# Kernel optimization log

Hardware: AMD Instinct MI355X
Metric: run time of the kernel (lower is better)

Reference implementation:

```python
import jax, jax.numpy as jnp
import numpy as np

L, KV, H, D, DM, F, V = 6, 1, 4, 256, 1152, 6912, 65536
HIST, T = 4095, 1
EPS = 1e-6


def setup_inputs():
    key = jax.random.key(0)
    ks = jax.random.split(key, 24)
    n = lambda k, s, sc=0.02: jax.random.normal(k, s, dtype=jnp.float32) * sc
    sf = D ** -0.25  # head_dim^-0.25 baked into q/k norm weights as in the source
    return {
        "input_ids": jax.random.randint(ks[0], (1, T), 0, V, dtype=jnp.int32),
        "attn_flag": 0,  # decode step: additive causal mask zeroed, as in the repo
        "key_cache": n(ks[1], (L, KV, D, HIST), 0.5),
        "value_cache": n(ks[2], (L, KV, HIST, D), 0.5),
        "embed_table": jax.random.randint(ks[3], (V, DM), 0, 256, dtype=jnp.int32),
        "embed_scale": jax.random.uniform(ks[4], (V, 1), minval=1e-4, maxval=1e-2, dtype=jnp.float32),
        "embed_zp": -jax.random.uniform(ks[5], (V, 1), minval=0.0, maxval=0.5, dtype=jnp.float32),
        "w_in_ln": 1.0 + n(ks[6], (L, DM)),
        "w_q_norm": (1.0 + n(ks[7], (L, D))) * sf,
        "w_k_norm": (1.0 + n(ks[8], (L, D))) * sf,
        "Wq": n(ks[9], (L, DM, H * D)),
        "Wk": n(ks[10], (L, DM, KV * D)),
        "Wv": n(ks[11], (L, DM, KV * D)),
        "Wo": n(ks[12], (L, H * D, DM)),
        "w_post_attn_ln": 1.0 + n(ks[13], (L, DM)),
        "w_pre_ffn_ln": 1.0 + n(ks[14], (L, DM)),
        "w_post_ffn_ln": 1.0 + n(ks[15], (L, DM)),
        "Wg": n(ks[16], (L, DM, F)),
        "Wu": n(ks[17], (L, DM, F)),
        "Wd": n(ks[18], (L, F, DM)),
        "w_final_norm": 1.0 + n(ks[19], (DM,)),
        "W_lm": n(ks[20], (DM, V)),
        "is_sliding": (jnp.arange(L) % 6) != 5,  # 5 local : 1 global pattern
    }


def _rms(x, w):
    return w * x / jnp.sqrt(jnp.mean(x * x, axis=-1, keepdims=True) + EPS)


def _rot_half(x, axis):
    x1, x2 = jnp.split(x, 2, axis=axis)
    return jnp.concatenate([-x2, x1], axis=axis)


def _rope(base, hist, S, d):
    pos = jnp.arange(hist, S, dtype=jnp.float32)[:, None]
    theta = base ** (-(jnp.arange(0, d, 2, dtype=jnp.float32) / d))
    ang = pos * theta
    c = jnp.concatenate([jnp.cos(ang)] * 2, axis=-1).astype(jnp.float16).astype(jnp.float32)
    s = jnp.concatenate([jnp.sin(ang)] * 2, axis=-1).astype(jnp.float16).astype(jnp.float32)
    return c, s  # (T, D), half-precision roundtrip mimics the .half() tables


def reference(input_ids, attn_flag, key_cache, value_cache, embed_table, embed_scale,
              embed_zp, w_in_ln, w_q_norm, w_k_norm, Wq, Wk, Wv, Wo, w_post_attn_ln,
              w_pre_ffn_ln, w_post_ffn_ln, Wg, Wu, Wd, w_final_norm, W_lm, is_sliding):
    Lc, KVc, Dd, hist = key_cache.shape
    Tq = input_ids.shape[1]
    S = hist + Tq
    Hh = Wq.shape[-1] // Dd
    G = Hh // KVc
    cos_g, sin_g = _rope(10000.0, hist, S, Dd)    # assigned to 'global' exactly as in source
    cos_l, sin_l = _rope(1000000.0, hist, S, Dd)  # assigned to 'local'
    mask = (jnp.arange(S)[None, :] > jnp.arange(Tq)[:, None]).astype(jnp.float32) * (-128.0 * float(attn_flag))  # (T,S)
    # int8-dequant embedding lookup: uint8 codes * per-row scale + per-row zero point
    h = embed_table[input_ids].astype(jnp.float32) * embed_scale[input_ids] + embed_zp[input_ids]  # (1,T,DM)

    def body(h, xs):
        ck, cv, slide, w_in, w_qn, w_kn, wq, wk, wv, wo, w_pa, w_pf, w_pof, wg, wu, wd = xs
        cq = jnp.where(slide, cos_l, cos_g)
        sq = jnp.where(slide, sin_l, sin_g)
        ckk, skk = cq.T, sq.T  # (D,T) for keys
        resid = h
        hn = _rms(h, w_in)                                                  # (1,T,DM)
        q = _rms((hn @ wq).reshape(Tq, Hh, Dd), w_qn).transpose(1, 0, 2)    # (H,T,D)
        k = _rms((hn @ wk).reshape(Tq, KVc, Dd), w_kn).transpose(1, 2, 0)   # (KV,D,T)
        v = (hn @ wv).reshape(Tq, KVc, Dd).transpose(1, 0, 2)               # (KV,T,D)
        q = q * cq + _rot_half(q, -1) * sq
        k = k * ckk[None] + _rot_half(k, 1) * skk[None]
        kf = jnp.concatenate([ck, k], axis=-1)   # (KV,D,S) new key cache
        vf = jnp.concatenate([cv, v], axis=1)    # (KV,S,D) new value cache
        kr = jnp.repeat(kf, G, axis=0)           # GQA repeat -> (H,D,S)
        vr = jnp.repeat(vf, G, axis=0)           # (H,S,D)
        attn = jax.nn.softmax(jnp.einsum('htd,hds->hts', q, kr) + mask[None], axis=-1)
        ao = jnp.einsum('hts,hsd->htd', attn, vr).transpose(1, 0, 2).reshape(1, Tq, Hh * Dd) @ wo
        h = resid + _rms(ao, w_pa)
        resid = h
        x = _rms(h, w_pf)
        m = (jax.nn.gelu(x @ wg, approximate=True) * (x @ wu)) @ wd
        h = resid + _rms(m, w_pof)
        return h, (kf, vf)

    h, (keys, values) = jax.lax.scan(
        body, h,
        (key_cache, value_cache, is_sliding, w_in_ln, w_q_norm, w_k_norm, Wq, Wk, Wv, Wo,
         w_post_attn_ln, w_pre_ffn_ln, w_post_ffn_ln, Wg, Wu, Wd))
    last = _rms(h[:, -1], w_final_norm)          # (1,DM)
    logits = last @ W_lm                          # (1,V)
    token = jnp.argmax(logits, axis=-1, keepdims=True).astype(jnp.int32)
    return keys, values, token
```

## Files before the change

kernel.cpp:

```cpp
#include <hip/hip_runtime.h>
#include <hip/hip_fp16.h>
#include <cmath>

#define LNUM 6
#define DM   1152
#define DHEAD 256
#define NH   4
#define FF   6912
#define VOC  65536
#define HIST 4095
#define SEQ  4096
#define EPSV 1e-6f

#define QKV_O 0
#define AP_O  9216
#define DP_O  16128
#define GU_O  23040
#define LG_O  105984
#define ZEND  171520
#define POP_O 171520
#define SPS_O 302592
#define HIN_O 303104
#define HM_O  310016
#define AMV_O 316928
#define AMI_O 317184

__device__ __forceinline__ float block_sum256(float v, float* red4) {
#pragma unroll
    for (int off = 32; off; off >>= 1) v += __shfl_xor(v, off);
    int t = threadIdx.x;
    if ((t & 63) == 0) red4[t >> 6] = v;
    __syncthreads();
    float r = red4[0] + red4[1] + red4[2] + red4[3];
    __syncthreads();
    return r;
}

__global__ __launch_bounds__(256) void gk_copy(const float* __restrict__ kc,
                                               const float* __restrict__ vc,
                                               float* __restrict__ keys,
                                               float* __restrict__ vals) {
    int b = blockIdx.x;
    if (b < 24576) {
        int row = b >> 4;
        int s = ((b & 15) << 8) + threadIdx.x;
        if (s < HIST) keys[(size_t)row * SEQ + s] = kc[(size_t)row * HIST + s];
    } else {
        int r = (b - 24576) * 4 + (threadIdx.x >> 6);
        int d4 = threadIdx.x & 63;
        if (r < LNUM * HIST) {
            int l = r / HIST, sI = r - l * HIST;
            ((float4*)(vals + ((size_t)l * SEQ + sI) * DHEAD))[d4] =
                ((const float4*)(vc + (size_t)r * DHEAD))[d4];
        }
    }
}

__global__ __launch_bounds__(256) void gk_qkv(
    const float* __restrict__ Wq, const float* __restrict__ Wk, const float* __restrict__ Wv,
    const float* __restrict__ w_in, const float* __restrict__ w_pof_prev,
    const float* __restrict__ hprev, const float* __restrict__ dprev,
    const int* __restrict__ ids, const int* __restrict__ tbl,
    const float* __restrict__ escale, const float* __restrict__ ezp,
    float* __restrict__ hin_out, float* __restrict__ qkv_out, int has_prev) {
    __shared__ float xv[DM];
    __shared__ float red4[4];
    __shared__ float4 qred[256];
    int t = threadIdx.x;
    if (has_prev) {
        float ss = 0.f;
        for (int i = t; i < DM; i += 256) { float d = dprev[i]; ss += d * d; }
        ss = block_sum256(ss, red4);
        float inv = 1.f / sqrtf(ss / DM + EPSV);
        for (int i = t; i < DM; i += 256)
            xv[i] = hprev[i] + w_pof_prev[i] * dprev[i] * inv;
    } else {
        int tok = ids[0];
        float sc = escale[tok], z = ezp[tok];
        const int* row = tbl + (size_t)tok * DM;
        for (int i = t; i < DM; i += 256) xv[i] = (float)row[i] * sc + z;
    }
    __syncthreads();
    if (blockIdx.x == 0 && blockIdx.y == 0)
        for (int i = t; i < DM; i += 256) hin_out[i] = xv[i];
    float ss = 0.f;
    for (int i = t; i < DM; i += 256) { float v = xv[i]; ss += v * v; }
    ss = block_sum256(ss, red4);
    float inv = 1.f / sqrtf(ss / DM + EPSV);
    for (int i = t; i < DM; i += 256) xv[i] = w_in[i] * xv[i] * inv;
    __syncthreads();

    int f4c = t & 63, ks = t >> 6;
    int jf = blockIdx.x * 64 + f4c;
    const float4* W4; int jj4, ncol4;
    if (jf < 256)      { W4 = (const float4*)Wq; jj4 = jf;       ncol4 = 256; }
    else if (jf < 320) { W4 = (const float4*)Wk; jj4 = jf - 256; ncol4 = 64; }
    else               { W4 = (const float4*)Wv; jj4 = jf - 320; ncol4 = 64; }
    int i0 = blockIdx.y * 64 + ks * 16;
    float4 w[16];
#pragma unroll
    for (int r = 0; r < 16; ++r) w[r] = W4[(size_t)(i0 + r) * ncol4 + jj4];
    float4 acc = {0, 0, 0, 0};
#pragma unroll
    for (int r = 0; r < 16; ++r) {
        float xs = xv[i0 + r];
        acc.x += xs * w[r].x; acc.y += xs * w[r].y;
        acc.z += xs * w[r].z; acc.w += xs * w[r].w;
    }
    qred[t] = acc;
    __syncthreads();
    if (ks == 0) {
        float4 a = qred[f4c], b = qred[64 + f4c], c = qred[128 + f4c], d = qred[192 + f4c];
        atomicAdd(&qkv_out[4 * jf + 0], a.x + b.x + c.x + d.x);
        atomicAdd(&qkv_out[4 * jf + 1], a.y + b.y + c.y + d.y);
        atomicAdd(&qkv_out[4 * jf + 2], a.z + b.z + c.z + d.z);
        atomicAdd(&qkv_out[4 * jf + 3], a.w + b.w + c.w + d.w);
    }
}

__global__ __launch_bounds__(256) void gk_attn(
    const float* __restrict__ qkv, const float* __restrict__ w_qn,
    const float* __restrict__ w_kn, const int* __restrict__ attn_flag,
    float* __restrict__ keys_l, float* __restrict__ vals_l,
    float* __restrict__ po_part, float* __restrict__ sum_part, float rope_base) {
    __shared__ float lq[NH * DHEAD];
    __shared__ float lqf[NH * DHEAD];
    __shared__ float lkn[DHEAD];
    __shared__ float lkf[DHEAD];
    __shared__ float lv[DHEAD];
    __shared__ float lp[NH * 32];
    __shared__ float red4[4];
    int t = threadIdx.x;
    int s0 = blockIdx.x * 32;
    bool last = (blockIdx.x == gridDim.x - 1);

    int jm = t & 127;
    float theta = powf(rope_base, -(float)(2 * jm) / 256.f);
    float ang = 4095.f * theta;
    float c = __half2float(__float2half(cosf(ang)));
    float s = __half2float(__float2half(sinf(ang)));

    for (int h = 0; h < NH; ++h) lq[h * 256 + t] = qkv[h * 256 + t];
    lkn[t] = qkv[1024 + t];
    lv[t]  = qkv[1280 + t];
    __syncthreads();
    for (int h = 0; h < NH; ++h) {
        float v = lq[h * 256 + t];
        float ss = block_sum256(v * v, red4);
        float inv = 1.f / sqrtf(ss / 256.f + EPSV);
        float qn = w_qn[t] * v * inv;
        lq[h * 256 + t] = qn;
        __syncthreads();
        float partner = (t < 128) ? -lq[h * 256 + t + 128] : lq[h * 256 + t - 128];
        lqf[h * 256 + t] = qn * c + partner * s;
    }
    {
        float v = lkn[t];
        float ss = block_sum256(v * v, red4);
        float inv = 1.f / sqrtf(ss / 256.f + EPSV);
        float kn = w_kn[t] * v * inv;
        lkn[t] = kn;
        __syncthreads();
        float partner = (t < 128) ? -lkn[t + 128] : lkn[t - 128];
        lkf[t] = kn * c + partner * s;
    }
    __syncthreads();
    if (last) {
        keys_l[(size_t)t * SEQ + (SEQ - 1)] = lkf[t];
        vals_l[(size_t)(SEQ - 1) * DHEAD + t] = lv[t];
    }
    int sl = t & 31, dc = t >> 5;
    int sg = s0 + sl;
    bool self = last && (sl == 31);
    float a0 = 0, a1 = 0, a2 = 0, a3 = 0;
#pragma unroll 4
    for (int dd = 0; dd < 32; ++dd) {
        int d = dc * 32 + dd;
        float kv = self ? lkf[d] : keys_l[(size_t)d * SEQ + sg];
        a0 += lqf[0 * 256 + d] * kv;
        a1 += lqf[1 * 256 + d] * kv;
        a2 += lqf[2 * 256 + d] * kv;
        a3 += lqf[3 * 256 + d] * kv;
    }
    __syncthreads();
    lq[0 * 256 + t] = a0; lq[1 * 256 + t] = a1; lq[2 * 256 + t] = a2; lq[3 * 256 + t] = a3;
    __syncthreads();
    if (t < 32) {
        int af = attn_flag[0];
        float mk = (s0 + t > 0) ? -128.f * (float)af : 0.f;
        for (int h = 0; h < NH; ++h) {
            float sc_ = 0.f;
#pragma unroll
            for (int d8 = 0; d8 < 8; ++d8) sc_ += lq[h * 256 + d8 * 32 + t];
            lp[h * 32 + t] = expf(sc_ + mk);
        }
    }
    __syncthreads();
    if (t < NH) {
        float su = 0.f;
        for (int i = 0; i < 32; ++i) su += lp[t * 32 + i];
        sum_part[blockIdx.x * NH + t] = su;
    }
    float p0 = 0, p1 = 0, p2 = 0, p3 = 0;
#pragma unroll 4
    for (int ss_ = 0; ss_ < 32; ++ss_) {
        float v = (last && ss_ == 31) ? lv[t] : vals_l[(size_t)(s0 + ss_) * DHEAD + t];
        p0 += lp[0 * 32 + ss_] * v;
        p1 += lp[1 * 32 + ss_] * v;
        p2 += lp[2 * 32 + ss_] * v;
        p3 += lp[3 * 32 + ss_] * v;
    }
    float* po = po_part + (size_t)blockIdx.x * NH * DHEAD;
    po[0 * 256 + t] = p0; po[1 * 256 + t] = p1; po[2 * 256 + t] = p2; po[3 * 256 + t] = p3;
}

__global__ __launch_bounds__(256) void gk_wo(
    const float* __restrict__ po_part, const float* __restrict__ sum_part,
    const float* __restrict__ Wo_l, float* __restrict__ aproj) {
    __shared__ float x[64];
    __shared__ float hinv[NH];
    __shared__ float red4[4];
    int t = threadIdx.x;
    for (int h = 0; h < NH; ++h) {
        float v = (t < 128) ? sum_part[t * NH + h] : 0.f;
        float tot = block_sum256(v, red4);
        if (t == 0) hinv[h] = 1.f / tot;
    }
    __syncthreads();
    int i0 = blockIdx.y * 64;
    if (t < 64) {
        float a = 0.f;
#pragma unroll 8
        for (int b = 0; b < 128; ++b) a += po_part[(size_t)b * 1024 + i0 + t];
        x[t] = a * hinv[(i0 + t) >> 8];
    }
    __syncthreads();
    int j = blockIdx.x * 256 + t;
    if (j < DM) {
        float acc = 0.f;
#pragma unroll 4
        for (int ii = 0; ii < 64; ++ii)
            acc += x[ii] * Wo_l[(size_t)(i0 + ii) * DM + j];
        atomicAdd(&aproj[j], acc);
    }
}

__global__ __launch_bounds__(256) void gk_gu(
    const float* __restrict__ Wg_l, const float* __restrict__ Wu_l,
    const float* __restrict__ w_pa, const float* __restrict__ w_pf,
    const float* __restrict__ hin, const float* __restrict__ aproj,
    float* __restrict__ hmid_out, float* __restrict__ gu_out) {
    __shared__ float xv[DM];
    __shared__ float red4[4];
    __shared__ float4 gred[256];
    int t = threadIdx.x;
    float ss = 0.f;
    for (int i = t; i < DM; i += 256) { float a = aproj[i]; ss += a * a; }
    ss = block_sum256(ss, red4);
    float inv = 1.f / sqrtf(ss / DM + EPSV);
    for (int i = t; i < DM; i += 256) xv[i] = hin[i] + w_pa[i] * aproj[i] * inv;
    __syncthreads();
    if (blockIdx.x == 0 && blockIdx.y == 0)
        for (int i = t; i < DM; i += 256) hmid_out[i] = xv[i];
    float s2 = 0.f;
    for (int i = t; i < DM; i += 256) { float v = xv[i]; s2 += v * v; }
    s2 = block_sum256(s2, red4);
    float inv2 = 1.f / sqrtf(s2 / DM + EPSV);
    for (int i = t; i < DM; i += 256) xv[i] = w_pf[i] * xv[i] * inv2;
    __syncthreads();

    int f4c = t & 63, ks = t >> 6;
    int cgi = blockIdx.x;
    bool isU = cgi >= 27;
    int cg = isU ? cgi - 27 : cgi;
    const float4* W4 = (const float4*)(isU ? Wu_l : Wg_l);
    int colf4 = cg * 64 + f4c;
    int i0 = blockIdx.y * 64 + ks * 16;
    float4 w[16];
#pragma unroll
    for (int r = 0; r < 16; ++r) w[r] = W4[(size_t)(i0 + r) * 1728 + colf4];
    float4 acc = {0, 0, 0, 0};
#pragma unroll
    for (int r = 0; r < 16; ++r) {
        float xs = xv[i0 + r];
        acc.x += xs * w[r].x; acc.y += xs * w[r].y;
        acc.z += xs * w[r].z; acc.w += xs * w[r].w;
    }
    gred[t] = acc;
    __syncthreads();
    if (ks == 0) {
        float4 a = gred[f4c], b = gred[64 + f4c], c = gred[128 + f4c], d = gred[192 + f4c];
        float* dst = gu_out + (isU ? FF : 0) + 4 * colf4;
        atomicAdd(dst + 0, a.x + b.x + c.x + d.x);
        atomicAdd(dst + 1, a.y + b.y + c.y + d.y);
        atomicAdd(dst + 2, a.z + b.z + c.z + d.z);
        atomicAdd(dst + 3, a.w + b.w + c.w + d.w);
    }
}

__global__ __launch_bounds__(256) void gk_wd(const float* __restrict__ gu,
                                             const float* __restrict__ Wd_l,
                                             float* __restrict__ dproj) {
    __shared__ float m[64];
    __shared__ float4 wred[256];
    int t = threadIdx.x;
    int i0 = blockIdx.y * 64;
    if (t < 64) {
        float g = gu[i0 + t], u = gu[FF + i0 + t];
        float gl = 0.5f * g * (1.f + tanhf(0.7978845608028654f * (g + 0.044715f * g * g * g)));
        m[t] = gl * u;
    }
    __syncthreads();
    int f4c = t & 63, ks = t >> 6;
    int col4 = blockIdx.x * 64 + f4c;
    float4 acc = {0, 0, 0, 0};
    if (col4 < 288) {
        const float4* W4 = (const float4*)Wd_l;
        float4 w[16];
#pragma unroll
        for (int r = 0; r < 16; ++r) w[r] = W4[(size_t)(i0 + ks * 16 + r) * 288 + col4];
#pragma unroll
        for (int r = 0; r < 16; ++r) {
            float xs = m[ks * 16 + r];
            acc.x += xs * w[r].x; acc.y += xs * w[r].y;
            acc.z += xs * w[r].z; acc.w += xs * w[r].w;
        }
    }
    wred[t] = acc;
    __syncthreads();
    if (ks == 0 && col4 < 288) {
        float4 a = wred[f4c], b = wred[64 + f4c], c = wred[128 + f4c], d = wred[192 + f4c];
        atomicAdd(&dproj[4 * col4 + 0], a.x + b.x + c.x + d.x);
        atomicAdd(&dproj[4 * col4 + 1], a.y + b.y + c.y + d.y);
        atomicAdd(&dproj[4 * col4 + 2], a.z + b.z + c.z + d.z);
        atomicAdd(&dproj[4 * col4 + 3], a.w + b.w + c.w + d.w);
    }
}

__global__ __launch_bounds__(256) void gk_logits(
    const float* __restrict__ W_lm, const float* __restrict__ w_pof5,
    const float* __restrict__ w_fin, const float* __restrict__ hmid5,
    const float* __restrict__ dproj5, float* __restrict__ lg) {
    __shared__ float xv[DM];
    __shared__ float red4[4];
    __shared__ float4 lred[256];
    int t = threadIdx.x;
    float ss = 0.f;
    for (int i = t; i < DM; i += 256) { float d = dproj5[i]; ss += d * d; }
    ss = block_sum256(ss, red4);
    float inv = 1.f / sqrtf(ss / DM + EPSV);
    for (int i = t; i < DM; i += 256) xv[i] = hmid5[i] + w_pof5[i] * dproj5[i] * inv;
    __syncthreads();
    float s2 = 0.f;
    for (int i = t; i < DM; i += 256) { float v = xv[i]; s2 += v * v; }
    s2 = block_sum256(s2, red4);
    float inv2 = 1.f / sqrtf(s2 / DM + EPSV);
    for (int i = t; i < DM; i += 256) xv[i] = w_fin[i] * xv[i] * inv2;
    __syncthreads();

    int f4c = t & 63, ks = t >> 6;
    int colf4 = blockIdx.x * 64 + f4c;
    int i0 = blockIdx.y * 64 + ks * 16;
    const float4* W4 = (const float4*)W_lm;
    float4 w[16];
#pragma unroll
    for (int r = 0; r < 16; ++r) w[r] = W4[(size_t)(i0 + r) * 16384 + colf4];
    float4 acc = {0, 0, 0, 0};
#pragma unroll
    for (int r = 0; r < 16; ++r) {
        float xs = xv[i0 + r];
        acc.x += xs * w[r].x; acc.y += xs * w[r].y;
        acc.z += xs * w[r].z; acc.w += xs * w[r].w;
    }
    lred[t] = acc;
    __syncthreads();
    if (ks == 0) {
        float4 a = lred[f4c], b = lred[64 + f4c], c = lred[128 + f4c], d = lred[192 + f4c];
        atomicAdd(&lg[4 * colf4 + 0], a.x + b.x + c.x + d.x);
        atomicAdd(&lg[4 * colf4 + 1], a.y + b.y + c.y + d.y);
        atomicAdd(&lg[4 * colf4 + 2], a.z + b.z + c.z + d.z);
        atomicAdd(&lg[4 * colf4 + 3], a.w + b.w + c.w + d.w);
    }
}

__global__ __launch_bounds__(256) void gk_amax1(const float* __restrict__ lg,
                                                float* __restrict__ pv, float* __restrict__ pi) {
    __shared__ float rv[256];
    __shared__ int ri[256];
    int t = threadIdx.x;
    int c = blockIdx.x * 256 + t;
    rv[t] = lg[c]; ri[t] = c;
    __syncthreads();
    for (int off = 128; off > 0; off >>= 1) {
        if (t < off) {
            float ov = rv[t + off]; int oi = ri[t + off];
            if (ov > rv[t] || (ov == rv[t] && oi < ri[t])) { rv[t] = ov; ri[t] = oi; }
        }
        __syncthreads();
    }
    if (t == 0) { pv[blockIdx.x] = rv[0]; pi[blockIdx.x] = (float)ri[0]; }
}

__global__ __launch_bounds__(256) void gk_amax2(const float* __restrict__ pv,
                                                const float* __restrict__ pi,
                                                float* __restrict__ tok_out) {
    __shared__ float rv[256];
    __shared__ int ri[256];
    int t = threadIdx.x;
    rv[t] = pv[t]; ri[t] = (int)pi[t];
    __syncthreads();
    for (int off = 128; off > 0; off >>= 1) {
        if (t < off) {
            float ov = rv[t + off]; int oi = ri[t + off];
            if (ov > rv[t] || (ov == rv[t] && oi < ri[t])) { rv[t] = ov; ri[t] = oi; }
        }
        __syncthreads();
    }
    if (t == 0) tok_out[0] = (float)ri[0];
}

extern "C" void kernel_launch(void* const* d_in, const int* in_sizes, int n_in,
                              void* d_out, int out_size, void* d_ws, size_t ws_size,
                              hipStream_t stream) {
    const int*   ids   = (const int*)d_in[0];
    const int*   aflag = (const int*)d_in[1];
    const float* kc    = (const float*)d_in[2];
    const float* vc    = (const float*)d_in[3];
    const int*   tbl   = (const int*)d_in[4];
    const float* esc   = (const float*)d_in[5];
    const float* ezp   = (const float*)d_in[6];
    const float* w_in  = (const float*)d_in[7];
    const float* w_qn  = (const float*)d_in[8];
    const float* w_kn  = (const float*)d_in[9];
    const float* Wq    = (const float*)d_in[10];
    const float* Wk    = (const float*)d_in[11];
    const float* Wv    = (const float*)d_in[12];
    const float* Wo    = (const float*)d_in[13];
    const float* w_pa  = (const float*)d_in[14];
    const float* w_pf  = (const float*)d_in[15];
    const float* w_pof = (const float*)d_in[16];
    const float* Wg    = (const float*)d_in[17];
    const float* Wu    = (const float*)d_in[18];
    const float* Wd    = (const float*)d_in[19];
    const float* w_fin = (const float*)d_in[20];
    const float* Wlm   = (const float*)d_in[21];

    float* keys = (float*)d_out;
    float* vals = keys + (size_t)LNUM * DHEAD * SEQ;
    float* tok  = vals + (size_t)LNUM * SEQ * DHEAD;
    float* ws = (float*)d_ws;

    hipMemsetAsync(ws, 0, ZEND * sizeof(float), stream);
    gk_copy<<<24576 + 6144, 256, 0, stream>>>(kc, vc, keys, vals);

    for (int l = 0; l < LNUM; ++l) {
        float* QKVl = ws + QKV_O + (size_t)l * 1536;
        float* APl  = ws + AP_O + (size_t)l * DM;
        float* DPl  = ws + DP_O + (size_t)l * DM;
        float* GUl  = ws + GU_O + (size_t)l * 2 * FF;
        float* HINl = ws + HIN_O + (size_t)l * DM;
        float* HMl  = ws + HM_O + (size_t)l * DM;
        float* keys_l = keys + (size_t)l * DHEAD * SEQ;
        float* vals_l = vals + (size_t)l * SEQ * DHEAD;

        gk_qkv<<<dim3(6, 18), 256, 0, stream>>>(
            Wq + (size_t)l * DM * 1024, Wk + (size_t)l * DM * 256,
            Wv + (size_t)l * DM * 256, w_in + (size_t)l * DM,
            w_pof + (size_t)(l ? l - 1 : 0) * DM,
            (l ? ws + HM_O + (size_t)(l - 1) * DM : nullptr),
            (l ? ws + DP_O + (size_t)(l - 1) * DM : nullptr),
            ids, tbl, esc, ezp, HINl, QKVl, (l > 0) ? 1 : 0);

        gk_attn<<<128, 256, 0, stream>>>(
            QKVl, w_qn + (size_t)l * DHEAD, w_kn + (size_t)l * DHEAD,
            aflag, keys_l, vals_l, ws + POP_O, ws + SPS_O,
            ((l % 6) != 5) ? 1000000.0f : 10000.0f);

        gk_wo<<<dim3(5, 16), 256, 0, stream>>>(
            ws + POP_O, ws + SPS_O, Wo + (size_t)l * 1024 * DM, APl);

        gk_gu<<<dim3(54, 18), 256, 0, stream>>>(
            Wg + (size_t)l * DM * FF, Wu + (size_t)l * DM * FF,
            w_pa + (size_t)l * DM, w_pf + (size_t)l * DM, HINl, APl, HMl, GUl);

        gk_wd<<<dim3(5, 108), 256, 0, stream>>>(GUl, Wd + (size_t)l * FF * DM, DPl);
    }

    gk_logits<<<dim3(256, 18), 256, 0, stream>>>(
        Wlm, w_pof + (size_t)5 * DM, w_fin,
        ws + HM_O + (size_t)5 * DM, ws + DP_O + (size_t)5 * DM, ws + LG_O);
    gk_amax1<<<256, 256, 0, stream>>>(ws + LG_O, ws + AMV_O, ws + AMI_O);
    gk_amax2<<<1, 256, 0, stream>>>(ws + AMV_O, ws + AMI_O, tok);
}
```

Measured before the change: 579.1 us.

## Fuse whole decode step into one cooperative persistent kernel with grid syncs

Replaces the sequence of about 33 kernel launches plus a memset with a single cooperative kernel of 256 blocks by 512 threads. Stages are separated by grid-wide barriers. The KV-cache copy for the next layer runs in idle blocks while attention executes, and the argmax is done with a packed 64-bit atomicMax. This removes launch gaps and lets the cache copy overlap compute. In exchange, every stage is limited to 256 blocks and pays grid-sync latency, and the old multi-kernel path is kept as a fallback if the cooperative launch fails.

```diff
diff --git a/kernel.cpp b/kernel.cpp
--- a/kernel.cpp
+++ b/kernel.cpp
@@ -1,6 +1,9 @@
 #include <hip/hip_runtime.h>
 #include <hip/hip_fp16.h>
+#include <hip/hip_cooperative_groups.h>
 #include <cmath>
+
+namespace cg = cooperative_groups;
 
 #define LNUM 6
 #define DM   1152
@@ -11,19 +14,477 @@
 #define HIST 4095
 #define SEQ  4096
 #define EPSV 1e-6f
+#define NB   256
+#define BS   512
 
 #define QKV_O 0
 #define AP_O  9216
 #define DP_O  16128
 #define GU_O  23040
 #define LG_O  105984
-#define ZEND  171520
-#define POP_O 171520
-#define SPS_O 302592
-#define HIN_O 303104
-#define HM_O  310016
-#define AMV_O 316928
-#define AMI_O 317184
+#define AMX_O 171520
+#define ZEND  171522
+#define POP_O 171528
+#define SPS_O 302600
+#define HIN_O 303112
+#define HM_O  310024
+#define AMV_O 316936
+#define AMI_O 317192
+
+struct P {
+    const int* ids; const int* aflag;
+    const float* kc; const float* vc;
+    const int* tbl; const float* esc; const float* ezp;
+    const float* w_in; const float* w_qn; const float* w_kn;
+    const float* Wq; const float* Wk; const float* Wv; const float* Wo;
+    const float* w_pa; const float* w_pf; const float* w_pof;
+    const float* Wg; const float* Wu; const float* Wd;
+    const float* w_fin; const float* Wlm;
+    float* keys; float* vals; float* tok; float* ws;
+};
+
+__device__ __forceinline__ float bsum512(float v, float* red8) {
+#pragma unroll
+    for (int off = 32; off; off >>= 1) v += __shfl_xor(v, off);
+    if ((threadIdx.x & 63) == 0) red8[threadIdx.x >> 6] = v;
+    __syncthreads();
+    float r = red8[0] + red8[1] + red8[2] + red8[3] +
+              red8[4] + red8[5] + red8[6] + red8[7];
+    __syncthreads();
+    return r;
+}
+
+__device__ __forceinline__ void copy_layer(const P& p, int l, int part) {
+    int t = threadIdx.x;
+#pragma unroll
+    for (int rr = 0; rr < 2; ++rr) {
+        int row = part * 2 + rr;
+        const float* src = p.kc + ((size_t)l * 256 + row) * HIST;
+        float* dst = p.keys + ((size_t)l * 256 + row) * SEQ;
+        for (int s = t; s < HIST; s += BS) dst[s] = src[s];
+    }
+    const float4* vc4 = (const float4*)p.vc;
+    float4* va4 = (float4*)p.vals;
+#pragma unroll
+    for (int rr = 0; rr < 4; ++rr) {
+        int s = part * 32 + rr * 8 + (t >> 6);
+        if (s < HIST)
+            va4[((size_t)l * SEQ + s) * 64 + (t & 63)] =
+                vc4[((size_t)l * HIST + s) * 64 + (t & 63)];
+    }
+}
+
+__global__ __launch_bounds__(BS) void mega(P p) {
+    cg::grid_group gg = cg::this_grid();
+    __shared__ float sm[5632];
+    const int t = threadIdx.x, bid = blockIdx.x;
+    float* ws = p.ws;
+
+    {
+        for (int g = bid * BS + t; g < ZEND; g += NB * BS) ws[g] = 0.f;
+        if (bid == 0) {
+            int tk = p.ids[0];
+            float sc = p.esc[tk], z = p.ezp[tk];
+            const int* row = p.tbl + (size_t)tk * DM;
+            for (int i = t; i < DM; i += BS) ws[HIN_O + i] = (float)row[i] * sc + z;
+        }
+        if (bid < 128) copy_layer(p, 0, bid);
+    }
+    gg.sync();
+
+    for (int l = 0; l < LNUM; ++l) {
+        float* QKV = ws + QKV_O + l * 1536;
+        float* AP  = ws + AP_O + l * DM;
+        float* DP  = ws + DP_O + l * DM;
+        float* GU  = ws + GU_O + l * 13824;
+        float* HIN = ws + HIN_O + l * DM;
+        float* HM  = ws + HM_O + l * DM;
+        float* POP = ws + POP_O;
+        float* SPS = ws + SPS_O;
+        float* keys_l = p.keys + (size_t)l * DHEAD * SEQ;
+        float* vals_l = p.vals + (size_t)l * SEQ * DHEAD;
+
+        {
+            float* xv = sm; float* red8 = sm + 1152;
+            float4* qred = (float4*)(sm + 1216);
+            if (l == 0) {
+                for (int i = t; i < DM; i += BS) xv[i] = ws[HIN_O + i];
+            } else {
+                const float* hprev = ws + HM_O + (l - 1) * DM;
+                const float* dprev = ws + DP_O + (l - 1) * DM;
+                const float* wpof = p.w_pof + (l - 1) * DM;
+                float ssd = 0.f;
+                for (int i = t; i < DM; i += BS) { float d = dprev[i]; ssd += d * d; }
+                ssd = bsum512(ssd, red8);
+                float inv = 1.f / sqrtf(ssd / DM + EPSV);
+                for (int i = t; i < DM; i += BS)
+                    xv[i] = hprev[i] + wpof[i] * dprev[i] * inv;
+            }
+            __syncthreads();
+            if (bid == 0) for (int i = t; i < DM; i += BS) HIN[i] = xv[i];
+            float ss2 = 0.f;
+            for (int i = t; i < DM; i += BS) { float v = xv[i]; ss2 += v * v; }
+            ss2 = bsum512(ss2, red8);
+            float inv2 = 1.f / sqrtf(ss2 / DM + EPSV);
+            const float* w_in = p.w_in + l * DM;
+            for (int i = t; i < DM; i += BS) xv[i] = w_in[i] * xv[i] * inv2;
+            __syncthreads();
+            if (bid < 96) {
+                int cg = bid % 6, kc = bid / 6;
+                int f4c = t & 63, ks = t >> 6;
+                int jf = cg * 64 + f4c;
+                const float4* W4; int jj4, nc4;
+                if (jf < 256)      { W4 = (const float4*)(p.Wq + (size_t)l * DM * 1024); jj4 = jf;       nc4 = 256; }
+                else if (jf < 320) { W4 = (const float4*)(p.Wk + (size_t)l * DM * 256);  jj4 = jf - 256; nc4 = 64; }
+                else               { W4 = (const float4*)(p.Wv + (size_t)l * DM * 256);  jj4 = jf - 320; nc4 = 64; }
+                int i0 = kc * 72 + ks * 9;
+                float4 w[9];
+#pragma unroll
+                for (int r = 0; r < 9; ++r) w[r] = W4[(size_t)(i0 + r) * nc4 + jj4];
+                float4 acc = {0, 0, 0, 0};
+#pragma unroll
+                for (int r = 0; r < 9; ++r) {
+                    float xs = xv[i0 + r];
+                    acc.x += xs * w[r].x; acc.y += xs * w[r].y;
+                    acc.z += xs * w[r].z; acc.w += xs * w[r].w;
+                }
+                qred[t] = acc;
+                __syncthreads();
+                if (ks == 0) {
+                    float sx = 0, sy = 0, sz = 0, sw = 0;
+#pragma unroll
+                    for (int k2 = 0; k2 < 8; ++k2) {
+                        float4 r = qred[k2 * 64 + f4c];
+                        sx += r.x; sy += r.y; sz += r.z; sw += r.w;
+                    }
+                    atomicAdd(&QKV[4 * jf + 0], sx); atomicAdd(&QKV[4 * jf + 1], sy);
+                    atomicAdd(&QKV[4 * jf + 2], sz); atomicAdd(&QKV[4 * jf + 3], sw);
+                }
+            }
+        }
+        gg.sync();
+
+        if (bid < 128) {
+            float* lq = sm;
+            float* lqf = sm + 1024;
+            float* lkn = sm + 2048;
+            float* lkf = sm + 2304;
+            float* lv  = sm + 2560;
+            float* lp  = sm + 2816;
+            float* red8 = sm + 2944;
+            float* scr = sm + 3072;
+            int s0 = bid * 32;
+            bool lastb = (bid == 127);
+            float base = ((l % 6) != 5) ? 1000000.f : 10000.f;
+            float c = 0.f, s = 0.f;
+            if (t < 256) {
+                int jm = t & 127;
+                float theta = powf(base, -(float)(2 * jm) / 256.f);
+                float ang = 4095.f * theta;
+                c = __half2float(__float2half(cosf(ang)));
+                s = __half2float(__float2half(sinf(ang)));
+                for (int h = 0; h < NH; ++h) lq[h * 256 + t] = QKV[h * 256 + t];
+                lkn[t] = QKV[1024 + t];
+                lv[t]  = QKV[1280 + t];
+            }
+            __syncthreads();
+            const float* wqn = p.w_qn + l * DHEAD;
+            const float* wkn = p.w_kn + l * DHEAD;
+            for (int h = 0; h < NH; ++h) {
+                float v = (t < 256) ? lq[h * 256 + t] : 0.f;
+                float ss = bsum512(v * v, red8);
+                float qn = 0.f;
+                if (t < 256) {
+                    qn = wqn[t] * v / sqrtf(ss / 256.f + EPSV);
+                    lq[h * 256 + t] = qn;
+                }
+                __syncthreads();
+                if (t < 256) {
+                    float partner = (t < 128) ? -lq[h * 256 + t + 128] : lq[h * 256 + t - 128];
+                    lqf[h * 256 + t] = qn * c + partner * s;
+                }
+                __syncthreads();
+            }
+            {
+                float v = (t < 256) ? lkn[t] : 0.f;
+                float ss = bsum512(v * v, red8);
+                float kn = 0.f;
+                if (t < 256) { kn = wkn[t] * v / sqrtf(ss / 256.f + EPSV); lkn[t] = kn; }
+                __syncthreads();
+                if (t < 256) {
+                    float pr = (t < 128) ? -lkn[t + 128] : lkn[t - 128];
+                    lkf[t] = kn * c + pr * s;
+                }
+                __syncthreads();
+            }
+            if (lastb && t < 256) {
+                keys_l[(size_t)t * SEQ + (SEQ - 1)] = lkf[t];
+                vals_l[(size_t)(SEQ - 1) * DHEAD + t] = lv[t];
+            }
+            int sl = t & 31, dc = t >> 5;
+            int sg = s0 + sl;
+            bool self = lastb && (sl == 31);
+            float a0 = 0, a1 = 0, a2 = 0, a3 = 0;
+#pragma unroll
+            for (int dd = 0; dd < 16; ++dd) {
+                int d = dc * 16 + dd;
+                float kv = self ? lkf[d] : keys_l[(size_t)d * SEQ + sg];
+                a0 += lqf[d] * kv; a1 += lqf[256 + d] * kv;
+                a2 += lqf[512 + d] * kv; a3 += lqf[768 + d] * kv;
+            }
+            scr[dc * 128 + sl]      = a0;
+            scr[dc * 128 + 32 + sl] = a1;
+            scr[dc * 128 + 64 + sl] = a2;
+            scr[dc * 128 + 96 + sl] = a3;
+            __syncthreads();
+            if (t < 128) {
+                int hh = t >> 5, si = t & 31;
+                int af = p.aflag[0];
+                float mk = (s0 + si > 0) ? -128.f * (float)af : 0.f;
+                float sc_ = 0.f;
+#pragma unroll
+                for (int d16 = 0; d16 < 16; ++d16) sc_ += scr[d16 * 128 + hh * 32 + si];
+                lp[hh * 32 + si] = expf(sc_ + mk);
+            }
+            __syncthreads();
+            if (t < NH) {
+                float su = 0.f;
+                for (int i = 0; i < 32; ++i) su += lp[t * 32 + i];
+                SPS[bid * NH + t] = su;
+            }
+            int f4 = t & 63, hp = (t >> 6) & 3, sr = t >> 8;
+            const float4* V4 = (const float4*)vals_l;
+            float4 acc = {0, 0, 0, 0};
+#pragma unroll
+            for (int ss_ = 0; ss_ < 16; ++ss_) {
+                int sI = sr * 16 + ss_;
+                float4 vv = (lastb && sI == 31) ? ((float4*)lv)[f4]
+                                                : V4[(size_t)(s0 + sI) * 64 + f4];
+                float pp = lp[hp * 32 + sI];
+                acc.x += pp * vv.x; acc.y += pp * vv.y;
+                acc.z += pp * vv.z; acc.w += pp * vv.w;
+            }
+            ((float4*)scr)[sr * 256 + hp * 64 + f4] = acc;
+            __syncthreads();
+            POP[(size_t)bid * 1024 + t]       = scr[t] + scr[1024 + t];
+            POP[(size_t)bid * 1024 + 512 + t] = scr[512 + t] + scr[1536 + t];
+        } else if (l + 1 < LNUM) {
+            copy_layer(p, l + 1, bid - 128);
+        }
+        gg.sync();
+
+        if (bid < 80) {
+            float* hinv = sm;
+            float* xl = sm + 8;
+            float* red8 = sm + 72;
+            float* wored = sm + 80;
+            int cgp = bid % 5, kc = bid / 5;
+            for (int h = 0; h < NH; ++h) {
+                float v = (t < 128) ? SPS[t * NH + h] : 0.f;
+                float tot = bsum512(v, red8);
+                if (t == 0) hinv[h] = 1.f / tot;
+            }
+            __syncthreads();
+            int i0 = kc * 64;
+            if (t < 64) {
+                float a = 0.f;
+#pragma unroll 8
+                for (int b = 0; b < 128; ++b) a += POP[(size_t)b * 1024 + i0 + t];
+                xl[t] = a * hinv[(i0 + t) >> 8];
+            }
+            __syncthreads();
+            const float* Wo_l = p.Wo + (size_t)l * 1024 * DM;
+            int j = cgp * 256 + (t & 255);
+            int kr = t >> 8;
+            float acc = 0.f;
+            if (j < DM) {
+#pragma unroll
+                for (int r = 0; r < 32; ++r) {
+                    int li = kr * 32 + r;
+                    acc += xl[li] * Wo_l[(size_t)(i0 + li) * DM + j];
+                }
+            }
+            wored[t] = acc;
+            __syncthreads();
+            if (t < 256 && j < DM) atomicAdd(&AP[j], wored[t] + wored[t + 256]);
+        }
+        gg.sync();
+
+        {
+            float* xv = sm; float* red8 = sm + 1152;
+            float4* gred = (float4*)(sm + 1216);
+            float ssa = 0.f;
+            for (int i = t; i < DM; i += BS) { float a = AP[i]; ssa += a * a; }
+            ssa = bsum512(ssa, red8);
+            float inv = 1.f / sqrtf(ssa / DM + EPSV);
+            const float* wpa = p.w_pa + l * DM;
+            for (int i = t; i < DM; i += BS) xv[i] = HIN[i] + wpa[i] * AP[i] * inv;
+            __syncthreads();
+            if (bid == 0) for (int i = t; i < DM; i += BS) HM[i] = xv[i];
+            float ssb = 0.f;
+            for (int i = t; i < DM; i += BS) { float v = xv[i]; ssb += v * v; }
+            ssb = bsum512(ssb, red8);
+            float inv2 = 1.f / sqrtf(ssb / DM + EPSV);
+            const float* wpf = p.w_pf + l * DM;
+            for (int i = t; i < DM; i += BS) xv[i] = wpf[i] * xv[i] * inv2;
+            __syncthreads();
+            int f4c = t & 63, ks = t >> 6;
+            for (int u = bid; u < 486; u += NB) {
+                int cgi = u % 54, kc = u / 54;
+                bool isU = cgi >= 27;
+                int cg = isU ? cgi - 27 : cgi;
+                const float4* W4 = (const float4*)((isU ? p.Wu : p.Wg) + (size_t)l * DM * FF);
+                int colf = cg * 64 + f4c;
+                int i0 = kc * 128 + ks * 16;
+                float4 w[16];
+#pragma unroll
+                for (int r = 0; r < 16; ++r) w[r] = W4[(size_t)(i0 + r) * 1728 + colf];
+                float4 acc = {0, 0, 0, 0};
+#pragma unroll
+                for (int r = 0; r < 16; ++r) {
+                    float xs = xv[i0 + r];
+                    acc.x += xs * w[r].x; acc.y += xs * w[r].y;
+                    acc.z += xs * w[r].z; acc.w += xs * w[r].w;
+                }
+                gred[t] = acc;
+                __syncthreads();
+                if (ks == 0) {
+                    float sx = 0, sy = 0, sz = 0, sw = 0;
+#pragma unroll
+                    for (int k2 = 0; k2 < 8; ++k2) {
+                        float4 r = gred[k2 * 64 + f4c];
+                        sx += r.x; sy += r.y; sz += r.z; sw += r.w;
+                    }
+                    float* dst = GU + (isU ? FF : 0) + 4 * colf;
+                    atomicAdd(dst + 0, sx); atomicAdd(dst + 1, sy);
+                    atomicAdd(dst + 2, sz); atomicAdd(dst + 3, sw);
+                }
+                __syncthreads();
+            }
+        }
+        gg.sync();
+
+        {
+            float* m = sm;
+            float4* wred = (float4*)(sm + 128);
+            const float4* Wd4 = (const float4*)(p.Wd + (size_t)l * FF * DM);
+            int f4c = t & 31, ks = t >> 5;
+            for (int u = bid; u < 486; u += NB) {
+                int cg = u % 9, kc = u / 9;
+                int i0 = kc * 128;
+                __syncthreads();
+                if (t < 128) {
+                    float g = GU[i0 + t], uu = GU[FF + i0 + t];
+                    float gl = 0.5f * g * (1.f + tanhf(0.7978845608028654f * (g + 0.044715f * g * g * g)));
+                    m[t] = gl * uu;
+                }
+                __syncthreads();
+                int col4 = cg * 32 + f4c;
+                float4 w[8];
+#pragma unroll
+                for (int r = 0; r < 8; ++r) w[r] = Wd4[(size_t)(i0 + ks * 8 + r) * 288 + col4];
+                float4 acc = {0, 0, 0, 0};
+#pragma unroll
+                for (int r = 0; r < 8; ++r) {
+                    float xs = m[ks * 8 + r];
+                    acc.x += xs * w[r].x; acc.y += xs * w[r].y;
+                    acc.z += xs * w[r].z; acc.w += xs * w[r].w;
+                }
+                wred[t] = acc;
+                __syncthreads();
+                if (t < 32) {
+                    float sx = 0, sy = 0, sz = 0, sw = 0;
+#pragma unroll
+                    for (int k2 = 0; k2 < 16; ++k2) {
+                        float4 r = wred[k2 * 32 + t];
+                        sx += r.x; sy += r.y; sz += r.z; sw += r.w;
+                    }
+                    int col4b = cg * 32 + t;
+                    atomicAdd(&DP[4 * col4b + 0], sx); atomicAdd(&DP[4 * col4b + 1], sy);
+                    atomicAdd(&DP[4 * col4b + 2], sz); atomicAdd(&DP[4 * col4b + 3], sw);
+                }
+            }
+        }
+        gg.sync();
+    }
+
+    {
+        float* xv = sm; float* red8 = sm + 1152;
+        float4* lred = (float4*)(sm + 1216);
+        const float* DP5 = ws + DP_O + 5 * DM;
+        const float* HM5 = ws + HM_O + 5 * DM;
+        const float* wpof5 = p.w_pof + 5 * DM;
+        float ss = 0.f;
+        for (int i = t; i < DM; i += BS) { float d = DP5[i]; ss += d * d; }
+        ss = bsum512(ss, red8);
+        float inv = 1.f / sqrtf(ss / DM + EPSV);
+        for (int i = t; i < DM; i += BS) xv[i] = HM5[i] + wpof5[i] * DP5[i] * inv;
+        __syncthreads();
+        float s2 = 0.f;
+        for (int i = t; i < DM; i += BS) { float v = xv[i]; s2 += v * v; }
+        s2 = bsum512(s2, red8);
+        float inv2 = 1.f / sqrtf(s2 / DM + EPSV);
+        for (int i = t; i < DM; i += BS) xv[i] = p.w_fin[i] * xv[i] * inv2;
+        __syncthreads();
+        const float4* W4 = (const float4*)p.Wlm;
+        float* LG = ws + LG_O;
+        int f4c = t & 63, ks = t >> 6;
+        for (int u = bid; u < 2048; u += NB) {
+            int cg = u & 255, kc = u >> 8;
+            int colf = cg * 64 + f4c;
+            int i0 = kc * 144 + ks * 18;
+            float4 w[18];
+#pragma unroll
+            for (int r = 0; r < 18; ++r) w[r] = W4[(size_t)(i0 + r) * 16384 + colf];
+            float4 acc = {0, 0, 0, 0};
+#pragma unroll
+            for (int r = 0; r < 18; ++r) {
+                float xs = xv[i0 + r];
+                acc.x += xs * w[r].x; acc.y += xs * w[r].y;
+                acc.z += xs * w[r].z; acc.w += xs * w[r].w;
+            }
+            lred[t] = acc;
+            __syncthreads();
+            if (ks == 0) {
+                float sx = 0, sy = 0, sz = 0, sw = 0;
+#pragma unroll
+                for (int k2 = 0; k2 < 8; ++k2) {
+                    float4 r = lred[k2 * 64 + f4c];
+                    sx += r.x; sy += r.y; sz += r.z; sw += r.w;
+                }
+                atomicAdd(&LG[4 * colf + 0], sx); atomicAdd(&LG[4 * colf + 1], sy);
+                atomicAdd(&LG[4 * colf + 2], sz); atomicAdd(&LG[4 * colf + 3], sw);
+            }
+            __syncthreads();
+        }
+    }
+    gg.sync();
+
+    {
+        unsigned long long* smu = (unsigned long long*)sm;
+        unsigned long long pk = 0;
+        if (t < 256) {
+            int c = bid * 256 + t;
+            float v = ws[LG_O + c];
+            unsigned bits = __float_as_uint(v);
+            unsigned key = (bits & 0x80000000u) ? ~bits : (bits | 0x80000000u);
+            pk = ((unsigned long long)key << 32) | (unsigned)(~c);
+        }
+        if (t < 256) smu[t] = pk;
+        __syncthreads();
+        for (int off = 128; off; off >>= 1) {
+            if (t < off) { if (smu[t + off] > smu[t]) smu[t] = smu[t + off]; }
+            __syncthreads();
+        }
+        if (t == 0) atomicMax((unsigned long long*)(ws + AMX_O), smu[0]);
+    }
+    gg.sync();
+    if (bid == 0 && t == 0) {
+        unsigned long long pk = *(unsigned long long*)(ws + AMX_O);
+        unsigned c = ~(unsigned)(pk & 0xFFFFFFFFull);
+        p.tok[0] = (float)c;
+    }
+}
 
 __device__ __forceinline__ float block_sum256(float v, float* red4) {
 #pragma unroll
@@ -89,7 +550,6 @@
     float inv = 1.f / sqrtf(ss / DM + EPSV);
     for (int i = t; i < DM; i += 256) xv[i] = w_in[i] * xv[i] * inv;
     __syncthreads();
-
     int f4c = t & 63, ks = t >> 6;
     int jf = blockIdx.x * 64 + f4c;
     const float4* W4; int jj4, ncol4;
@@ -133,13 +593,11 @@
     int t = threadIdx.x;
     int s0 = blockIdx.x * 32;
     bool last = (blockIdx.x == gridDim.x - 1);
-
     int jm = t & 127;
     float theta = powf(rope_base, -(float)(2 * jm) / 256.f);
     float ang = 4095.f * theta;
     float c = __half2float(__float2half(cosf(ang)));
     float s = __half2float(__float2half(sinf(ang)));
-
     for (int h = 0; h < NH; ++h) lq[h * 256 + t] = qkv[h * 256 + t];
     lkn[t] = qkv[1024 + t];
     lv[t]  = qkv[1280 + t];
@@ -268,7 +726,6 @@
     float inv2 = 1.f / sqrtf(s2 / DM + EPSV);
     for (int i = t; i < DM; i += 256) xv[i] = w_pf[i] * xv[i] * inv2;
     __syncthreads();
-
     int f4c = t & 63, ks = t >> 6;
     int cgi = blockIdx.x;
     bool isU = cgi >= 27;
@@ -357,7 +814,6 @@
     float inv2 = 1.f / sqrtf(s2 / DM + EPSV);
     for (int i = t; i < DM; i += 256) xv[i] = w_fin[i] * xv[i] * inv2;
     __syncthreads();
-
     int f4c = t & 63, ks = t >> 6;
     int colf4 = blockIdx.x * 64 + f4c;
     int i0 = blockIdx.y * 64 + ks * 16;
@@ -422,73 +878,77 @@
 extern "C" void kernel_launch(void* const* d_in, const int* in_sizes, int n_in,
                               void* d_out, int out_size, void* d_ws, size_t ws_size,
                               hipStream_t stream) {
-    const int*   ids   = (const int*)d_in[0];
-    const int*   aflag = (const int*)d_in[1];
-    const float* kc    = (const float*)d_in[2];
-    const float* vc    = (const float*)d_in[3];
-    const int*   tbl   = (const int*)d_in[4];
-    const float* esc   = (const float*)d_in[5];
-    const float* ezp   = (const float*)d_in[6];
-    const float* w_in  = (const float*)d_in[7];
-    const float* w_qn  = (const float*)d_in[8];
-    const float* w_kn  = (const float*)d_in[9];
-    const float* Wq    = (const float*)d_in[10];
-    const float* Wk    = (const float*)d_in[11];
-    const float* Wv    = (const float*)d_in[12];
-    const float* Wo    = (const float*)d_in[13];
-    const float* w_pa  = (const float*)d_in[14];
-    const float* w_pf  = (const float*)d_in[15];
-    const float* w_pof = (const float*)d_in[16];
-    const float* Wg    = (const float*)d_in[17];
-    const float* Wu    = (const float*)d_in[18];
-    const float* Wd    = (const float*)d_in[19];
-    const float* w_fin = (const float*)d_in[20];
-    const float* Wlm   = (const float*)d_in[21];
-
-    float* keys = (float*)d_out;
-    float* vals = keys + (size_t)LNUM * DHEAD * SEQ;
-    float* tok  = vals + (size_t)LNUM * SEQ * DHEAD;
+    P p;
+    p.ids   = (const int*)d_in[0];
+    p.aflag = (const int*)d_in[1];
+    p.kc    = (const float*)d_in[2];
+    p.vc    = (const float*)d_in[3];
+    p.tbl   = (const int*)d_in[4];
+    p.esc   = (const float*)d_in[5];
+    p.ezp   = (const float*)d_in[6];
+    p.w_in  = (const float*)d_in[7];
+    p.w_qn  = (const float*)d_in[8];
+    p.w_kn  = (const float*)d_in[9];
+    p.Wq    = (const float*)d_in[10];
+    p.Wk    = (const float*)d_in[11];
+    p.Wv    = (const float*)d_in[12];
+    p.Wo    = (const float*)d_in[13];
+    p.w_pa  = (const float*)d_in[14];
+    p.w_pf  = (const float*)d_in[15];
+    p.w_pof = (const float*)d_in[16];
+    p.Wg    = (const float*)d_in[17];
+    p.Wu    = (const float*)d_in[18];
+    p.Wd    = (const float*)d_in[19];
+    p.w_fin = (const float*)d_in[20];
+    p.Wlm   = (const float*)d_in[21];
+    p.keys  = (float*)d_out;
+    p.vals  = p.keys + (size_t)LNUM * DHEAD * SEQ;
+    p.tok   = p.vals + (size_t)LNUM * SEQ * DHEAD;
+    p.ws    = (float*)d_ws;
     float* ws = (float*)d_ws;
 
-    hipMemsetAsync(ws, 0, ZEND * sizeof(float), stream);
-    gk_copy<<<24576 + 6144, 256, 0, stream>>>(kc, vc, keys, vals);
-
-    for (int l = 0; l < LNUM; ++l) {
-        float* QKVl = ws + QKV_O + (size_t)l * 1536;
-        float* APl  = ws + AP_O + (size_t)l * DM;
-        float* DPl  = ws + DP_O + (size_t)l * DM;
-        float* GUl  = ws + GU_O + (size_t)l * 2 * FF;
-        float* HINl = ws + HIN_O + (size_t)l * DM;
-        float* HMl  = ws + HM_O + (size_t)l * DM;
-        float* keys_l = keys + (size_t)l * DHEAD * SEQ;
-        float* vals_l = vals + (size_t)l * SEQ * DHEAD;
-
-        gk_qkv<<<dim3(6, 18), 256, 0, stream>>>(
-            Wq + (size_t)l * DM * 1024, Wk + (size_t)l * DM * 256,
-            Wv + (size_t)l * DM * 256, w_in + (size_t)l * DM,
-            w_pof + (size_t)(l ? l - 1 : 0) * DM,
-            (l ? ws + HM_O + (size_t)(l - 1) * DM : nullptr),
-            (l ? ws + DP_O + (size_t)(l - 1) * DM : nullptr),
-            ids, tbl, esc, ezp, HINl, QKVl, (l > 0) ? 1 : 0);
-
-        gk_attn<<<128, 256, 0, stream>>>(
-            QKVl, w_qn + (size_t)l * DHEAD, w_kn + (size_t)l * DHEAD,
-            aflag, keys_l, vals_l, ws + POP_O, ws + SPS_O,
-            ((l % 6) != 5) ? 1000000.0f : 10000.0f);
-
-        gk_wo<<<dim3(5, 16), 256, 0, stream>>>(
-            ws + POP_O, ws + SPS_O, Wo + (size_t)l * 1024 * DM, APl);
-
-        gk_gu<<<dim3(54, 18), 256, 0, stream>>>(
-            Wg + (size_t)l * DM * FF, Wu + (size_t)l * DM * FF,
-            w_pa + (size_t)l * DM, w_pf + (size_t)l * DM, HINl, APl, HMl, GUl);
-
-        gk_wd<<<dim3(5, 108), 256, 0, stream>>>(GUl, Wd + (size_t)l * FF * DM, DPl);
-    }
-
-    gk_logits<<<dim3(256, 18), 256, 0, stream>>>(
-        Wlm, w_pof + (size_t)5 * DM, w_fin,
-        ws + HM_O + (size_t)5 * DM, ws + DP_O + (size_t)5 * DM, ws + LG_O);
-    gk_amax1<<<256, 256, 0, stream>>>(ws + LG_O, ws + AMV_O, ws + AMI_O);
-    gk_amax2<<<1, 256, 0, stream>>>(ws + AMV_O, ws + AMI_O, tok);
-}
+    void* args[] = { &p };
+    hipError_t err = hipLaunchCooperativeKernel((void*)mega, dim3(NB), dim3(BS), args, 0, stream);
+
+    if (err != hipSuccess) {
+        hipMemsetAsync(ws, 0, ZEND * sizeof(float), stream);
+        gk_copy<<<24576 + 6144, 256, 0, stream>>>(p.kc, p.vc, p.keys, p.vals);
+        for (int l = 0; l < LNUM; ++l) {
+            float* QKVl = ws + QKV_O + (size_t)l * 1536;
+            float* APl  = ws + AP_O + (size_t)l * DM;
+            float* DPl  = ws + DP_O + (size_t)l * DM;
+            float* GUl  = ws + GU_O + (size_t)l * 2 * FF;
+            float* HINl = ws + HIN_O + (size_t)l * DM;
+            float* HMl  = ws + HM_O + (size_t)l * DM;
+            float* keys_l = p.keys + (size_t)l * DHEAD * SEQ;
+            float* vals_l = p.vals + (size_t)l * SEQ * DHEAD;
+
+            gk_qkv<<<dim3(6, 18), 256, 0, stream>>>(
+                p.Wq + (size_t)l * DM * 1024, p.Wk + (size_t)l * DM * 256,
+                p.Wv + (size_t)l * DM * 256, p.w_in + (size_t)l * DM,
+                p.w_pof + (size_t)(l ? l - 1 : 0) * DM,
+                (l ? ws + HM_O + (size_t)(l - 1) * DM : nullptr),
+                (l ? ws + DP_O + (size_t)(l - 1) * DM : nullptr),
+                p.ids, p.tbl, p.esc, p.ezp, HINl, QKVl, (l > 0) ? 1 : 0);
+
+            gk_attn<<<128, 256, 0, stream>>>(
+                QKVl, p.w_qn + (size_t)l * DHEAD, p.w_kn + (size_t)l * DHEAD,
+                p.aflag, keys_l, vals_l, ws + POP_O, ws + SPS_O,
+                ((l % 6) != 5) ? 1000000.0f : 10000.0f);
+
+            gk_wo<<<dim3(5, 16), 256, 0, stream>>>(
+                ws + POP_O, ws + SPS_O, p.Wo + (size_t)l * 1024 * DM, APl);
+
+            gk_gu<<<dim3(54, 18), 256, 0, stream>>>(
+                p.Wg + (size_t)l * DM * FF, p.Wu + (size_t)l * DM * FF,
+                p.w_pa + (size_t)l * DM, p.w_pf + (size_t)l * DM, HINl, APl, HMl, GUl);
+
+            gk_wd<<<dim3(5, 108), 256, 0, stream>>>(GUl, p.Wd + (size_t)l * FF * DM, DPl);
+        }
+        gk_logits<<<dim3(256, 18), 256, 0, stream>>>(
+            p.Wlm, p.w_pof + (size_t)5 * DM, p.w_fin,
+            ws + HM_O + (size_t)5 * DM, ws + DP_O + (size_t)5 * DM, ws + LG_O);
+        gk_amax1<<<256, 256, 0, stream>>>(ws + LG_O, ws + AMV_O, ws + AMI_O);
+        gk_amax2<<<1, 256, 0, stream>>>(ws + AMV_O, ws + AMI_O, p.tok);
+    }
+}
```

New measurement: 1.550 ms. 2.68x slower.
